# Performance work log

Hardware: AMD Instinct MI355X
Metric: run time of the kernel (lower is better)

The kernel has to match this reference:

```python
import jax, jax.numpy as jnp
import numpy as np

N_NODES = 50000
EPS_BN = 1e-5


def _glorot(key, shape):
    fan_in, fan_out = shape[0], shape[1]
    lim = jnp.sqrt(6.0 / (fan_in + fan_out))
    return jax.random.uniform(key, shape, jnp.float32, -lim, lim)


def setup_inputs() -> dict:
    key = jax.random.key(0)
    ks = jax.random.split(key, 12)
    x = jax.random.normal(ks[0], (N_NODES, 128), jnp.float32)
    y = jax.random.normal(ks[1], (256, 1), jnp.float32)
    edge_index = jax.random.randint(ks[2], (2, 800000), 0, N_NODES, jnp.int64)
    return {
        "x": x,
        "y": y,
        "edge_index": edge_index,
        # GCNConv weights (in_dim, out_dim) + bias
        "W1": _glorot(ks[3], (128, 128)), "b1": jnp.zeros((128,), jnp.float32),
        "W2": _glorot(ks[4], (128, 128)), "b2": jnp.zeros((128,), jnp.float32),
        "W3": _glorot(ks[5], (128, 64)),  "b3": jnp.zeros((64,), jnp.float32),
        # target MLP: BatchNorm1d(1) -> Linear(1,128) -> ReLU -> Dropout -> Linear(128,64)
        "bn_gamma": jnp.ones((1,), jnp.float32), "bn_beta": jnp.zeros((1,), jnp.float32),
        "Wm1": _glorot(ks[6], (1, 128)),  "bm1": jnp.zeros((128,), jnp.float32),
        "Wm2": _glorot(ks[7], (128, 64)), "bm2": jnp.zeros((64,), jnp.float32),
    }


def gcn_conv(h, W, b, src, dst, deg_isqrt, n):
    # PyG GCNConv: x' = D^-1/2 (A+I) D^-1/2 (x W) + b, self-loops included in src/dst
    h = h @ W  # [n, out]
    norm = (deg_isqrt[src] * deg_isqrt[dst])[:, None]  # [E, 1]
    msg = h[src] * norm  # gather + scale, [E, out]
    out = jax.ops.segment_sum(msg, dst, num_segments=n)  # scatter-add
    return out + b


def reference(x, y, edge_index, W1, b1, W2, b2, W3, b3, bn_gamma, bn_beta, Wm1, bm1, Wm2, bm2):
    n = x.shape[0]
    loops = jnp.arange(n, dtype=edge_index.dtype)
    src = jnp.concatenate([edge_index[0], loops])
    dst = jnp.concatenate([edge_index[1], loops])
    deg = jax.ops.segment_sum(jnp.ones_like(dst, dtype=x.dtype), dst, num_segments=n)
    deg_isqrt = jnp.where(deg > 0, jax.lax.rsqrt(deg), 0.0)

    h = jax.nn.relu(gcn_conv(x, W1, b1, src, dst, deg_isqrt, n))
    h = jax.nn.relu(gcn_conv(h, W2, b2, src, dst, deg_isqrt, n))
    h = gcn_conv(h, W3, b3, src, dst, deg_isqrt, n)
    # transform_feat: normalize per-node embeddings (global_mean_pool result is discarded in source)
    x_emb = h / jnp.clip(jnp.linalg.norm(h, axis=1, keepdims=True), 1e-12)

    # target branch: BatchNorm1d (training-mode batch stats), Linear, ReLU, Dropout(eval=id), Linear
    mu = jnp.mean(y, axis=0, keepdims=True)
    var = jnp.var(y, axis=0, keepdims=True)
    yb = (y - mu) * jax.lax.rsqrt(var + EPS_BN) * bn_gamma + bn_beta
    t = jax.nn.relu(yb @ Wm1 + bm1)
    t = t @ Wm2 + bm2
    y_emb = t / jnp.clip(jnp.linalg.norm(t, axis=1, keepdims=True), 1e-12)
    return (x_emb, y_emb)
```

## Files before the change

kernel.cpp:

```cpp
#include <hip/hip_runtime.h>
#include <hip/hip_bf16.h>

typedef __attribute__((ext_vector_type(8))) short short8;
typedef __attribute__((ext_vector_type(4))) float f32x4;

__device__ __forceinline__ ushort f2bf(float f) {
    union { float f; uint u; } v; v.f = f;
    uint u = v.u;
    return (ushort)((u + 0x7fffu + ((u >> 16) & 1u)) >> 16);
}
__device__ __forceinline__ float bf_lo(uint u) { return __uint_as_float(u << 16); }
__device__ __forceinline__ float bf_hi(uint u) { return __uint_as_float(u & 0xffff0000u); }
__device__ __forceinline__ float lane_bcast_f(float v, int j) {
    return __uint_as_float(__builtin_amdgcn_readlane(__float_as_uint(v), j));
}

#define PCHUNK 4096

__global__ __launch_bounds__(256) void k_partition(const int* __restrict__ src,
                                                   const int* __restrict__ dst, int E,
                                                   int nbuck, int cap,
                                                   int* __restrict__ gcur,
                                                   uint* __restrict__ part) {
    __shared__ int hist[256];
    __shared__ int base[256];
    __shared__ int cnt2[256];
    const int tid = threadIdx.x;
    const int s0 = blockIdx.x * PCHUNK;
    const int send = min(s0 + PCHUNK, E);
    hist[tid] = 0;
    cnt2[tid] = 0;
    __syncthreads();
    for (int i = s0 + tid; i < send; i += 256) {
        int d = dst[i];
        atomicAdd(&hist[d >> 8], 1);
    }
    __syncthreads();
    if (tid < nbuck && hist[tid] > 0) base[tid] = atomicAdd(&gcur[tid], hist[tid]);
    __syncthreads();
    for (int i = s0 + tid; i < send; i += 256) {
        int d = dst[i];
        int s = src[i];
        int k = d >> 8;
        int r = base[k] + atomicAdd(&cnt2[k], 1);
        if (r < cap) part[(size_t)k * cap + r] = ((uint)d << 16) | (uint)s;
    }
}

__global__ void k_bucketscan(const int* __restrict__ gcur, int nbuck, int* __restrict__ bstart) {
    __shared__ int sm[256];
    int tid = threadIdx.x;
    int v = (tid < nbuck) ? gcur[tid] : 0;
    sm[tid] = v;
    __syncthreads();
    for (int off = 1; off < 256; off <<= 1) {
        int t = (tid >= off) ? sm[tid - off] : 0;
        __syncthreads();
        sm[tid] += t;
        __syncthreads();
    }
    if (tid < nbuck) bstart[tid] = sm[tid] - v;
    if (tid == nbuck - 1) bstart[nbuck] = sm[tid];
}

__global__ __launch_bounds__(256) void k_bucket_sort(const uint* __restrict__ part,
                                                     const int* __restrict__ gcur,
                                                     const int* __restrict__ bstart,
                                                     int cap, int n,
                                                     int* __restrict__ rowptr,
                                                     float* __restrict__ dis,
                                                     int* __restrict__ csr) {
    __shared__ int hist[256];
    __shared__ int pfx[256];
    const int b = blockIdx.x;
    const int tid = threadIdx.x;
    int sz = gcur[b];
    if (sz > cap) sz = cap;
    const uint* seg = part + (size_t)b * cap;
    const int outbase = bstart[b];

    hist[tid] = 0;
    __syncthreads();
    for (int i = tid; i < sz; i += 256) atomicAdd(&hist[(seg[i] >> 16) & 255], 1);
    __syncthreads();

    int cnt_t = hist[tid];
    pfx[tid] = cnt_t;
    __syncthreads();
    for (int off = 1; off < 256; off <<= 1) {
        int t = (tid >= off) ? pfx[tid - off] : 0;
        __syncthreads();
        pfx[tid] += t;
        __syncthreads();
    }
    int excl = pfx[tid] - cnt_t;

    int node = b * 256 + tid;
    if (node < n) {
        rowptr[node] = outbase + excl;
        dis[node] = rsqrtf((float)(cnt_t + 1));
        if (node == n - 1) rowptr[n] = outbase + excl + cnt_t;
    }
    __syncthreads();
    pfx[tid] = excl;
    hist[tid] = 0;
    __syncthreads();
    for (int i = tid; i < sz; i += 256) {
        uint p = seg[i];
        int j = (p >> 16) & 255;
        int r = atomicAdd(&hist[j], 1);
        csr[outbase + pfx[j] + r] = (int)(p & 0xffffu);
    }
}

__global__ void k_ew(const int* __restrict__ csr, const float* __restrict__ dis,
                     float* __restrict__ ew, int E) {
    int i = blockIdx.x * 256 + threadIdx.x;
    if (i < E) ew[i] = dis[csr[i]];
}

__global__ void k_xcast(const float* __restrict__ X, ushort* __restrict__ Xb, int n4) {
    int i = blockIdx.x * 256 + threadIdx.x;
    if (i < n4) {
        float4 v = ((const float4*)X)[i];
        ushort4 o;
        o.x = f2bf(v.x); o.y = f2bf(v.y); o.z = f2bf(v.z); o.w = f2bf(v.w);
        ((ushort4*)Xb)[i] = o;
    }
}

__global__ void k_wcast(const float* __restrict__ W, ushort* __restrict__ Wt, int N) {
    int i = blockIdx.x * 256 + threadIdx.x;
    if (i < 128 * N) {
        int k = i / N, nn = i - k * N;
        Wt[nn * 128 + k] = f2bf(W[i]);
    }
}

template <int COLS>
__global__ __launch_bounds__(256) void gemm_mfma(const ushort* __restrict__ Xb,
                                                 const ushort* __restrict__ Wt,
                                                 ushort* __restrict__ Y, int n) {
    constexpr int LDW = 136;
    __shared__ ushort sX[64 * LDW];
    __shared__ ushort sW[COLS * LDW];
    const int tid = threadIdx.x;
    const int row0 = blockIdx.x * 64;

#pragma unroll
    for (int c = tid; c < 64 * 16; c += 256) {
        int r = c >> 4, kc = c & 15;
        int gr = min(row0 + r, n - 1);
        uint4 v = *(const uint4*)&Xb[(size_t)gr * 128 + kc * 8];
        *(uint4*)&sX[r * LDW + kc * 8] = v;
    }
#pragma unroll
    for (int c = tid; c < COLS * 16; c += 256) {
        int r = c >> 4, kc = c & 15;
        uint4 v = *(const uint4*)&Wt[(size_t)r * 128 + kc * 8];
        *(uint4*)&sW[r * LDW + kc * 8] = v;
    }
    __syncthreads();

    constexpr int NT = (COLS == 128) ? 2 : 1;
    constexpr int WN = COLS / 4;
    const int w = tid >> 6;
    const int lane = tid & 63;
    const int lm = lane & 15;
    const int kq = lane >> 4;

    f32x4 acc[4][NT];
#pragma unroll
    for (int mt = 0; mt < 4; ++mt)
#pragma unroll
        for (int ntn = 0; ntn < NT; ++ntn) acc[mt][ntn] = (f32x4){0.f, 0.f, 0.f, 0.f};

#pragma unroll
    for (int ks = 0; ks < 4; ++ks) {
        const int k0 = ks * 32 + kq * 8;
        short8 bfr[NT];
#pragma unroll
        for (int ntn = 0; ntn < NT; ++ntn)
            bfr[ntn] = *(const short8*)&sW[(w * WN + ntn * 16 + lm) * LDW + k0];
#pragma unroll
        for (int mt = 0; mt < 4; ++mt) {
            short8 afr = *(const short8*)&sX[(mt * 16 + lm) * LDW + k0];
#pragma unroll
            for (int ntn = 0; ntn < NT; ++ntn)
                acc[mt][ntn] = __builtin_amdgcn_mfma_f32_16x16x32_bf16(afr, bfr[ntn], acc[mt][ntn], 0, 0, 0);
        }
    }

#pragma unroll
    for (int mt = 0; mt < 4; ++mt) {
        int r_base = row0 + mt * 16 + kq * 4;
#pragma unroll
        for (int ntn = 0; ntn < NT; ++ntn) {
            int col = w * WN + ntn * 16 + lm;
#pragma unroll
            for (int rr = 0; rr < 4; ++rr) {
                int r = r_base + rr;
                if (r < n) Y[(size_t)r * COLS + col] = f2bf(acc[mt][ntn][rr]);
            }
        }
    }
}

template <int COLS, bool RELU, bool NORM>
__global__ __launch_bounds__(256) void agg(const ushort* __restrict__ H,
                                           const float* __restrict__ dis,
                                           const int* __restrict__ rowptr,
                                           const int* __restrict__ csr,
                                           const float* __restrict__ ew,
                                           const float* __restrict__ bias,
                                           void* __restrict__ out, int n) {
    const int wid = blockIdx.x * 4 + (threadIdx.x >> 6);
    const int lane = threadIdx.x & 63;
    if (wid >= n) return;
    const int v = wid;
    const float dv = dis[v];
    const int e0 = rowptr[v];
    const int e1 = rowptr[v + 1];

    if (COLS == 128) {
        const uint* Hu = (const uint*)H;
        uint h0 = Hu[(size_t)v * 64 + lane];
        float ax = dv * bf_lo(h0), ay = dv * bf_hi(h0);

        int e = e0;
        while (e < e1) {
            const int c = min(e1 - e, 64);
            int sidx = 0; float sw = 0.0f;
            if (lane < c) { sidx = csr[e + lane]; sw = ew[e + lane]; }
            int j = 0;
            for (; j + 8 <= c; j += 8) {
                uint hv[8]; float w[8];
#pragma unroll
                for (int u = 0; u < 8; ++u) {
                    int s = __builtin_amdgcn_readlane(sidx, j + u);
                    w[u] = lane_bcast_f(sw, j + u);
                    hv[u] = Hu[(size_t)s * 64 + lane];
                }
#pragma unroll
                for (int u = 0; u < 8; ++u) { ax += w[u] * bf_lo(hv[u]); ay += w[u] * bf_hi(hv[u]); }
            }
            for (; j + 4 <= c; j += 4) {
                uint hv[4]; float w[4];
#pragma unroll
                for (int u = 0; u < 4; ++u) {
                    int s = __builtin_amdgcn_readlane(sidx, j + u);
                    w[u] = lane_bcast_f(sw, j + u);
                    hv[u] = Hu[(size_t)s * 64 + lane];
                }
#pragma unroll
                for (int u = 0; u < 4; ++u) { ax += w[u] * bf_lo(hv[u]); ay += w[u] * bf_hi(hv[u]); }
            }
            for (; j < c; ++j) {
                int s = __builtin_amdgcn_readlane(sidx, j);
                float w = lane_bcast_f(sw, j);
                uint hh = Hu[(size_t)s * 64 + lane];
                ax += w * bf_lo(hh); ay += w * bf_hi(hh);
            }
            e += c;
        }

        float2 b = ((const float2*)bias)[lane];
        float rx = dv * ax + b.x;
        float ry = dv * ay + b.y;
        if (RELU) { rx = fmaxf(rx, 0.f); ry = fmaxf(ry, 0.f); }
        uint packed = (uint)f2bf(rx) | ((uint)f2bf(ry) << 16);
        ((uint*)out)[(size_t)v * 64 + lane] = packed;
    } else {
        float acc = dv * bf_lo((uint)H[(size_t)v * 64 + lane]);

        int e = e0;
        while (e < e1) {
            const int c = min(e1 - e, 64);
            int sidx = 0; float sw = 0.0f;
            if (lane < c) { sidx = csr[e + lane]; sw = ew[e + lane]; }
            int j = 0;
            for (; j + 8 <= c; j += 8) {
                ushort hv[8]; float w[8];
#pragma unroll
                for (int u = 0; u < 8; ++u) {
                    int s = __builtin_amdgcn_readlane(sidx, j + u);
                    w[u] = lane_bcast_f(sw, j + u);
                    hv[u] = H[(size_t)s * 64 + lane];
                }
#pragma unroll
                for (int u = 0; u < 8; ++u) acc += w[u] * bf_lo((uint)hv[u]);
            }
            for (; j < c; ++j) {
                int s = __builtin_amdgcn_readlane(sidx, j);
                float w = lane_bcast_f(sw, j);
                acc += w * bf_lo((uint)H[(size_t)s * 64 + lane]);
            }
            e += c;
        }

        float r = dv * acc + bias[lane];
        if (RELU) r = fmaxf(r, 0.f);
        if (NORM) {
            float ss = r * r;
#pragma unroll
            for (int m = 1; m < 64; m <<= 1) ss += __shfl_xor(ss, m, 64);
            r = r / fmaxf(sqrtf(ss), 1e-12f);
        }
        ((float*)out)[(size_t)v * 64 + lane] = r;
    }
}

__global__ __launch_bounds__(256) void target_mlp(const float* __restrict__ y,
                                                  const float* __restrict__ gamma,
                                                  const float* __restrict__ beta,
                                                  const float* __restrict__ Wm1,
                                                  const float* __restrict__ bm1,
                                                  const float* __restrict__ Wm2,
                                                  const float* __restrict__ bm2,
                                                  float* __restrict__ out) {
    __shared__ float red[256];
    __shared__ float t1[128];
    __shared__ float s_mu, s_var;
    const int tid = threadIdx.x;
    float yv = y[tid];
    red[tid] = yv;
    __syncthreads();
    for (int s = 128; s > 0; s >>= 1) {
        if (tid < s) red[tid] += red[tid + s];
        __syncthreads();
    }
    if (tid == 0) s_mu = red[0] * (1.0f / 256.0f);
    __syncthreads();
    float mu = s_mu;
    float d = yv - mu;
    red[tid] = d * d;
    __syncthreads();
    for (int s = 128; s > 0; s >>= 1) {
        if (tid < s) red[tid] += red[tid + s];
        __syncthreads();
    }
    if (tid == 0) s_var = red[0] * (1.0f / 256.0f);
    __syncthreads();

    const int row = blockIdx.x;
    float yb = (y[row] - mu) * rsqrtf(s_var + 1e-5f) * gamma[0] + beta[0];
    if (tid < 128) t1[tid] = fmaxf(yb * Wm1[tid] + bm1[tid], 0.0f);
    __syncthreads();
    if (tid < 64) {
        float acc = bm2[tid];
#pragma unroll 8
        for (int c = 0; c < 128; ++c) acc += t1[c] * Wm2[c * 64 + tid];
        float ss = acc * acc;
#pragma unroll
        for (int m = 1; m < 64; m <<= 1) ss += __shfl_xor(ss, m, 64);
        out[row * 64 + tid] = acc / fmaxf(sqrtf(ss), 1e-12f);
    }
}

extern "C" void kernel_launch(void* const* d_in, const int* in_sizes, int n_in,
                              void* d_out, int out_size, void* d_ws, size_t ws_size,
                              hipStream_t stream) {
    const float* x     = (const float*)d_in[0];
    const float* y     = (const float*)d_in[1];
    const int*   edge  = (const int*)d_in[2];
    const float* W1    = (const float*)d_in[3];
    const float* b1    = (const float*)d_in[4];
    const float* W2    = (const float*)d_in[5];
    const float* b2    = (const float*)d_in[6];
    const float* W3    = (const float*)d_in[7];
    const float* b3    = (const float*)d_in[8];
    const float* bng   = (const float*)d_in[9];
    const float* bnb   = (const float*)d_in[10];
    const float* Wm1   = (const float*)d_in[11];
    const float* bm1   = (const float*)d_in[12];
    const float* Wm2   = (const float*)d_in[13];
    const float* bm2   = (const float*)d_in[14];

    const int n = in_sizes[0] / 128;
    const int E = in_sizes[2] / 2;
    const int* src = edge;
    const int* dst = edge + E;

    const int nbuck = (n + 255) / 256;
    const int cap = E / nbuck + E / nbuck / 4 + 1024;

    size_t off = 0;
    auto carve = [&](size_t bytes) {
        size_t p = off;
        off = (off + bytes + 255) & ~(size_t)255;
        return p;
    };
    char* ws = (char*)d_ws;
    int*    gcur    = (int*)(ws + carve(256 * 4));
    int*    bstart  = (int*)(ws + carve(257 * 4));
    uint*   part    = (uint*)(ws + carve((size_t)nbuck * cap * 4));
    int*    rowptr  = (int*)(ws + carve((size_t)(n + 1) * 4));
    int*    csr     = (int*)(ws + carve((size_t)E * 4));
    float*  ew      = (float*)(ws + carve((size_t)E * 4));
    float*  dis     = (float*)(ws + carve((size_t)n * 4));
    ushort* xb      = (ushort*)(ws + carve((size_t)n * 128 * 2));
    ushort* wt1     = (ushort*)(ws + carve(128 * 128 * 2));
    ushort* wt2     = (ushort*)(ws + carve(128 * 128 * 2));
    ushort* wt3     = (ushort*)(ws + carve(64 * 128 * 2));
    ushort* bufA    = (ushort*)(ws + carve((size_t)n * 128 * 2));
    ushort* bufB    = (ushort*)(ws + carve((size_t)n * 128 * 2));
    ushort* bufC    = (ushort*)(ws + carve((size_t)n * 64 * 2));
    (void)ws_size; (void)n_in; (void)out_size;

    float* x_emb = (float*)d_out;
    float* y_emb = (float*)d_out + (size_t)n * 64;

    hipMemsetAsync(gcur, 0, 256 * 4, stream);
    k_partition<<<(E + PCHUNK - 1) / PCHUNK, 256, 0, stream>>>(src, dst, E, nbuck, cap, gcur, part);
    k_bucketscan<<<1, 256, 0, stream>>>(gcur, nbuck, bstart);
    k_bucket_sort<<<nbuck, 256, 0, stream>>>(part, gcur, bstart, cap, n, rowptr, dis, csr);
    k_ew<<<(E + 255) / 256, 256, 0, stream>>>(csr, dis, ew, E);

    k_xcast<<<((n * 128 / 4) + 255) / 256, 256, 0, stream>>>(x, xb, n * 128 / 4);
    k_wcast<<<(128 * 128 + 255) / 256, 256, 0, stream>>>(W1, wt1, 128);
    k_wcast<<<(128 * 128 + 255) / 256, 256, 0, stream>>>(W2, wt2, 128);
    k_wcast<<<(128 * 64 + 255) / 256, 256, 0, stream>>>(W3, wt3, 64);

    const int ggrid = (n + 63) / 64;
    const int agrid = (n + 3) / 4;

    gemm_mfma<128><<<ggrid, 256, 0, stream>>>(xb, wt1, bufA, n);
    agg<128, true, false><<<agrid, 256, 0, stream>>>(bufA, dis, rowptr, csr, ew, b1, bufB, n);
    gemm_mfma<128><<<ggrid, 256, 0, stream>>>(bufB, wt2, bufA, n);
    agg<128, true, false><<<agrid, 256, 0, stream>>>(bufA, dis, rowptr, csr, ew, b2, bufB, n);
    gemm_mfma<64><<<ggrid, 256, 0, stream>>>(bufB, wt3, bufC, n);
    agg<64, false, true><<<agrid, 256, 0, stream>>>(bufC, dis, rowptr, csr, ew, b3, x_emb, n);

    target_mlp<<<256, 256, 0, stream>>>(y, bng, bnb, Wm1, bm1, Wm2, bm2, y_emb);
}
```

Baseline: 280.3 us.

## Fuse preprocessing kernels and compute edge weights on the fly in aggregation

Folds the bucket prefix scan into each bucket-sort block, merges the three weight-cast kernels into one launch, and fuses the fp32-to-bf16 cast of x into the first GEMM's shared-memory load. It also drops the precomputed per-edge weight array, so aggregation now gathers dis[src] directly, and it widens the aggregation unroll from 8 to 16 edges. The goal is fewer kernel launches and less intermediate global traffic. The costs are redundant scans in every bucket-sort block, an extra dependent gather per edge in aggregation, and more registers from the larger unroll.

After: 268.7 us. -4.1%, faster.

```diff
diff --git a/kernel.cpp b/kernel.cpp
--- a/kernel.cpp
+++ b/kernel.cpp
@@ -47,37 +47,30 @@
     }
 }
 
-__global__ void k_bucketscan(const int* __restrict__ gcur, int nbuck, int* __restrict__ bstart) {
-    __shared__ int sm[256];
-    int tid = threadIdx.x;
-    int v = (tid < nbuck) ? gcur[tid] : 0;
-    sm[tid] = v;
-    __syncthreads();
-    for (int off = 1; off < 256; off <<= 1) {
-        int t = (tid >= off) ? sm[tid - off] : 0;
-        __syncthreads();
-        sm[tid] += t;
-        __syncthreads();
-    }
-    if (tid < nbuck) bstart[tid] = sm[tid] - v;
-    if (tid == nbuck - 1) bstart[nbuck] = sm[tid];
-}
-
 __global__ __launch_bounds__(256) void k_bucket_sort(const uint* __restrict__ part,
                                                      const int* __restrict__ gcur,
-                                                     const int* __restrict__ bstart,
-                                                     int cap, int n,
+                                                     int nbuck, int cap, int n,
                                                      int* __restrict__ rowptr,
                                                      float* __restrict__ dis,
                                                      int* __restrict__ csr) {
     __shared__ int hist[256];
     __shared__ int pfx[256];
+    __shared__ int sscan[256];
     const int b = blockIdx.x;
     const int tid = threadIdx.x;
-    int sz = gcur[b];
-    if (sz > cap) sz = cap;
+
+    int gv = (tid < nbuck) ? min(gcur[tid], cap) : 0;
+    sscan[tid] = gv;
+    __syncthreads();
+    for (int off = 1; off < 256; off <<= 1) {
+        int t = (tid >= off) ? sscan[tid - off] : 0;
+        __syncthreads();
+        sscan[tid] += t;
+        __syncthreads();
+    }
+    const int outbase = (b == 0) ? 0 : sscan[b - 1];
+    const int sz = min(gcur[b], cap);
     const uint* seg = part + (size_t)b * cap;
-    const int outbase = bstart[b];
 
     hist[tid] = 0;
     __syncthreads();
@@ -113,32 +106,27 @@
     }
 }
 
-__global__ void k_ew(const int* __restrict__ csr, const float* __restrict__ dis,
-                     float* __restrict__ ew, int E) {
+__global__ void k_wcast3(const float* __restrict__ W1, const float* __restrict__ W2,
+                         const float* __restrict__ W3,
+                         ushort* __restrict__ wt1, ushort* __restrict__ wt2,
+                         ushort* __restrict__ wt3) {
     int i = blockIdx.x * 256 + threadIdx.x;
-    if (i < E) ew[i] = dis[csr[i]];
-}
-
-__global__ void k_xcast(const float* __restrict__ X, ushort* __restrict__ Xb, int n4) {
-    int i = blockIdx.x * 256 + threadIdx.x;
-    if (i < n4) {
-        float4 v = ((const float4*)X)[i];
-        ushort4 o;
-        o.x = f2bf(v.x); o.y = f2bf(v.y); o.z = f2bf(v.z); o.w = f2bf(v.w);
-        ((ushort4*)Xb)[i] = o;
-    }
-}
-
-__global__ void k_wcast(const float* __restrict__ W, ushort* __restrict__ Wt, int N) {
-    int i = blockIdx.x * 256 + threadIdx.x;
-    if (i < 128 * N) {
-        int k = i / N, nn = i - k * N;
-        Wt[nn * 128 + k] = f2bf(W[i]);
-    }
-}
-
-template <int COLS>
-__global__ __launch_bounds__(256) void gemm_mfma(const ushort* __restrict__ Xb,
+    if (i < 16384) {
+        int k = i >> 7, nn = i & 127;
+        wt1[nn * 128 + k] = f2bf(W1[i]);
+    } else if (i < 32768) {
+        int j = i - 16384;
+        int k = j >> 7, nn = j & 127;
+        wt2[nn * 128 + k] = f2bf(W2[j]);
+    } else if (i < 40960) {
+        int j = i - 32768;
+        int k = j >> 6, nn = j & 63;
+        wt3[nn * 128 + k] = f2bf(W3[j]);
+    }
+}
+
+template <int COLS, bool F32IN>
+__global__ __launch_bounds__(256) void gemm_mfma(const void* __restrict__ Xin,
                                                  const ushort* __restrict__ Wt,
                                                  ushort* __restrict__ Y, int n) {
     constexpr int LDW = 136;
@@ -147,12 +135,28 @@
     const int tid = threadIdx.x;
     const int row0 = blockIdx.x * 64;
 
-#pragma unroll
-    for (int c = tid; c < 64 * 16; c += 256) {
-        int r = c >> 4, kc = c & 15;
-        int gr = min(row0 + r, n - 1);
-        uint4 v = *(const uint4*)&Xb[(size_t)gr * 128 + kc * 8];
-        *(uint4*)&sX[r * LDW + kc * 8] = v;
+    if (F32IN) {
+        const float* Xf = (const float*)Xin;
+#pragma unroll
+        for (int i = 0; i < 8; ++i) {
+            int idx = i * 256 + tid;
+            int r = idx >> 5, kc = idx & 31;
+            int gr = min(row0 + r, n - 1);
+            float4 v = *(const float4*)&Xf[(size_t)gr * 128 + kc * 4];
+            ushort4 o;
+            o.x = f2bf(v.x); o.y = f2bf(v.y); o.z = f2bf(v.z); o.w = f2bf(v.w);
+            *(ushort4*)&sX[r * LDW + kc * 4] = o;
+        }
+    } else {
+        const ushort* Xb = (const ushort*)Xin;
+#pragma unroll
+        for (int i = 0; i < 4; ++i) {
+            int idx = i * 256 + tid;
+            int r = idx >> 4, kc = idx & 15;
+            int gr = min(row0 + r, n - 1);
+            uint4 v = *(const uint4*)&Xb[(size_t)gr * 128 + kc * 8];
+            *(uint4*)&sX[r * LDW + kc * 8] = v;
+        }
     }
 #pragma unroll
     for (int c = tid; c < COLS * 16; c += 256) {
@@ -211,7 +215,6 @@
                                            const float* __restrict__ dis,
                                            const int* __restrict__ rowptr,
                                            const int* __restrict__ csr,
-                                           const float* __restrict__ ew,
                                            const float* __restrict__ bias,
                                            void* __restrict__ out, int n) {
     const int wid = blockIdx.x * 4 + (threadIdx.x >> 6);
@@ -231,18 +234,18 @@
         while (e < e1) {
             const int c = min(e1 - e, 64);
             int sidx = 0; float sw = 0.0f;
-            if (lane < c) { sidx = csr[e + lane]; sw = ew[e + lane]; }
+            if (lane < c) { sidx = csr[e + lane]; sw = dis[sidx]; }
             int j = 0;
-            for (; j + 8 <= c; j += 8) {
-                uint hv[8]; float w[8];
-#pragma unroll
-                for (int u = 0; u < 8; ++u) {
+            for (; j + 16 <= c; j += 16) {
+                uint hv[16]; float w[16];
+#pragma unroll
+                for (int u = 0; u < 16; ++u) {
                     int s = __builtin_amdgcn_readlane(sidx, j + u);
                     w[u] = lane_bcast_f(sw, j + u);
                     hv[u] = Hu[(size_t)s * 64 + lane];
                 }
 #pragma unroll
-                for (int u = 0; u < 8; ++u) { ax += w[u] * bf_lo(hv[u]); ay += w[u] * bf_hi(hv[u]); }
+                for (int u = 0; u < 16; ++u) { ax += w[u] * bf_lo(hv[u]); ay += w[u] * bf_hi(hv[u]); }
             }
             for (; j + 4 <= c; j += 4) {
                 uint hv[4]; float w[4];
@@ -277,18 +280,18 @@
         while (e < e1) {
             const int c = min(e1 - e, 64);
             int sidx = 0; float sw = 0.0f;
-            if (lane < c) { sidx = csr[e + lane]; sw = ew[e + lane]; }
+            if (lane < c) { sidx = csr[e + lane]; sw = dis[sidx]; }
             int j = 0;
-            for (; j + 8 <= c; j += 8) {
-                ushort hv[8]; float w[8];
-#pragma unroll
-                for (int u = 0; u < 8; ++u) {
+            for (; j + 16 <= c; j += 16) {
+                ushort hv[16]; float w[16];
+#pragma unroll
+                for (int u = 0; u < 16; ++u) {
                     int s = __builtin_amdgcn_readlane(sidx, j + u);
                     w[u] = lane_bcast_f(sw, j + u);
                     hv[u] = H[(size_t)s * 64 + lane];
                 }
 #pragma unroll
-                for (int u = 0; u < 8; ++u) acc += w[u] * bf_lo((uint)hv[u]);
+                for (int u = 0; u < 16; ++u) acc += w[u] * bf_lo((uint)hv[u]);
             }
             for (; j < c; ++j) {
                 int s = __builtin_amdgcn_readlane(sidx, j);
@@ -392,13 +395,10 @@
     };
     char* ws = (char*)d_ws;
     int*    gcur    = (int*)(ws + carve(256 * 4));
-    int*    bstart  = (int*)(ws + carve(257 * 4));
     uint*   part    = (uint*)(ws + carve((size_t)nbuck * cap * 4));
     int*    rowptr  = (int*)(ws + carve((size_t)(n + 1) * 4));
     int*    csr     = (int*)(ws + carve((size_t)E * 4));
-    float*  ew      = (float*)(ws + carve((size_t)E * 4));
     float*  dis     = (float*)(ws + carve((size_t)n * 4));
-    ushort* xb      = (ushort*)(ws + carve((size_t)n * 128 * 2));
     ushort* wt1     = (ushort*)(ws + carve(128 * 128 * 2));
     ushort* wt2     = (ushort*)(ws + carve(128 * 128 * 2));
     ushort* wt3     = (ushort*)(ws + carve(64 * 128 * 2));
@@ -412,24 +412,18 @@
 
     hipMemsetAsync(gcur, 0, 256 * 4, stream);
     k_partition<<<(E + PCHUNK - 1) / PCHUNK, 256, 0, stream>>>(src, dst, E, nbuck, cap, gcur, part);
-    k_bucketscan<<<1, 256, 0, stream>>>(gcur, nbuck, bstart);
-    k_bucket_sort<<<nbuck, 256, 0, stream>>>(part, gcur, bstart, cap, n, rowptr, dis, csr);
-    k_ew<<<(E + 255) / 256, 256, 0, stream>>>(csr, dis, ew, E);
-
-    k_xcast<<<((n * 128 / 4) + 255) / 256, 256, 0, stream>>>(x, xb, n * 128 / 4);
-    k_wcast<<<(128 * 128 + 255) / 256, 256, 0, stream>>>(W1, wt1, 128);
-    k_wcast<<<(128 * 128 + 255) / 256, 256, 0, stream>>>(W2, wt2, 128);
-    k_wcast<<<(128 * 64 + 255) / 256, 256, 0, stream>>>(W3, wt3, 64);
+    k_bucket_sort<<<nbuck, 256, 0, stream>>>(part, gcur, nbuck, cap, n, rowptr, dis, csr);
+    k_wcast3<<<160, 256, 0, stream>>>(W1, W2, W3, wt1, wt2, wt3);
 
     const int ggrid = (n + 63) / 64;
     const int agrid = (n + 3) / 4;
 
-    gemm_mfma<128><<<ggrid, 256, 0, stream>>>(xb, wt1, bufA, n);
-    agg<128, true, false><<<agrid, 256, 0, stream>>>(bufA, dis, rowptr, csr, ew, b1, bufB, n);
-    gemm_mfma<128><<<ggrid, 256, 0, stream>>>(bufB, wt2, bufA, n);
-    agg<128, true, false><<<agrid, 256, 0, stream>>>(bufA, dis, rowptr, csr, ew, b2, bufB, n);
-    gemm_mfma<64><<<ggrid, 256, 0, stream>>>(bufB, wt3, bufC, n);
-    agg<64, false, true><<<agrid, 256, 0, stream>>>(bufC, dis, rowptr, csr, ew, b3, x_emb, n);
+    gemm_mfma<128, true><<<ggrid, 256, 0, stream>>>(x, wt1, bufA, n);
+    agg<128, true, false><<<agrid, 256, 0, stream>>>(bufA, dis, rowptr, csr, b1, bufB, n);
+    gemm_mfma<128, false><<<ggrid, 256, 0, stream>>>(bufB, wt2, bufA, n);
+    agg<128, true, false><<<agrid, 256, 0, stream>>>(bufA, dis, rowptr, csr, b2, bufB, n);
+    gemm_mfma<64, false><<<ggrid, 256, 0, stream>>>(bufB, wt3, bufC, n);
+    agg<64, false, true><<<agrid, 256, 0, stream>>>(bufC, dis, rowptr, csr, b3, x_emb, n);
 
     target_mlp<<<256, 256, 0, stream>>>(y, bng, bnb, Wm1, bm1, Wm2, bm2, y_emb);
 }
```
